# Optimization experiments

Hardware: AMD Instinct MI355X
Metric: run time of the kernel (lower is better)

## Reference

```python
import jax, jax.numpy as jnp
import numpy as np

N_NODES = 8192
N_EDGES = 131072

_DIMS = [
    ("cnn1", 3, 32), ("cnn2", 32, 64), ("cnn3", 64, 128),
    ("gcn1", 128, 256), ("gcn2", 256, 512), ("gcn3", 512, 1024),
    ("cnnd1", 1024, 512), ("cnnd2", 512, 256), ("cnnd3", 256, 128), ("cnnd4", 128, 50),
]


def setup_inputs() -> dict:
    key = jax.random.key(0)
    ks = jax.random.split(key, 2 + 2 * len(_DIMS))
    inp = {
        "x": jax.random.normal(ks[0], (N_NODES, 3), dtype=jnp.float32),
        "edge_index": jax.random.randint(ks[1], (2, N_EDGES), 0, N_NODES, dtype=jnp.int64)
        if jax.config.jax_enable_x64 else
        jax.random.randint(ks[1], (2, N_EDGES), 0, N_NODES, dtype=jnp.int32),
    }
    for i, (name, din, dout) in enumerate(_DIMS):
        scale = 1.0 / np.sqrt(din)
        inp[name + "_w"] = jax.random.normal(ks[2 + 2 * i], (din, dout), dtype=jnp.float32) * scale
        inp[name + "_b"] = jax.random.normal(ks[3 + 2 * i], (dout,), dtype=jnp.float32) * scale
    return inp


def _gcn_norm(edge_index, n, dtype):
    # add self-loops, symmetric normalization D^{-1/2}(A+I)D^{-1/2}
    loop = jnp.arange(n, dtype=edge_index.dtype)
    src = jnp.concatenate([edge_index[0], loop])
    dst = jnp.concatenate([edge_index[1], loop])
    deg = jax.ops.segment_sum(jnp.ones_like(dst, dtype=dtype), dst, num_segments=n)
    dinv = jnp.where(deg > 0, 1.0 / jnp.sqrt(deg), 0.0)
    norm = dinv[src] * dinv[dst]  # [E+N]
    return src, dst, norm


def _forward(x, edge_index,
             cnn1_w, cnn1_b, cnn2_w, cnn2_b, cnn3_w, cnn3_b,
             gcn1_w, gcn1_b, gcn2_w, gcn2_b, gcn3_w, gcn3_b,
             cnnd1_w, cnnd1_b, cnnd2_w, cnnd2_b, cnnd3_w, cnnd3_b, cnnd4_w, cnnd4_b):
    n = x.shape[0]
    src, dst, norm = _gcn_norm(edge_index, n, x.dtype)

    def lin(h, w, b):  # 1x1 Conv1d == per-node linear
        return h @ w + b

    def gcn(h, w, b):
        hl = h @ w                                    # [N, out]
        msg = hl[src] * norm[:, None]                 # gather + scale [E+N, out]
        return jax.ops.segment_sum(msg, dst, num_segments=n) + b

    h = jax.nn.relu(lin(x, cnn1_w, cnn1_b))
    h = jax.nn.relu(lin(h, cnn2_w, cnn2_b))
    h = jax.nn.relu(lin(h, cnn3_w, cnn3_b))
    h = jax.nn.relu(gcn(h, gcn1_w, gcn1_b))
    h = jax.nn.relu(gcn(h, gcn2_w, gcn2_b))
    h = jax.nn.relu(gcn(h, gcn3_w, gcn3_b))
    h = jax.nn.relu(lin(h, cnnd1_w, cnnd1_b))
    h = jax.nn.relu(lin(h, cnnd2_w, cnnd2_b))
    h = jax.nn.relu(lin(h, cnnd3_w, cnnd3_b))
    h = lin(h, cnnd4_w, cnnd4_b)
    return jax.nn.softmax(h, axis=1)  # [N, output_dim]


def reference(x, edge_index,
              cnn1_w, cnn1_b, cnn2_w, cnn2_b, cnn3_w, cnn3_b,
              gcn1_w, gcn1_b, gcn2_w, gcn2_b, gcn3_w, gcn3_b,
              cnnd1_w, cnnd1_b, cnnd2_w, cnnd2_b, cnnd3_w, cnnd3_b, cnnd4_w, cnnd4_b):
    return _forward(x, edge_index,
                    cnn1_w, cnn1_b, cnn2_w, cnn2_b, cnn3_w, cnn3_b,
                    gcn1_w, gcn1_b, gcn2_w, gcn2_b, gcn3_w, gcn3_b,
                    cnnd1_w, cnnd1_b, cnnd2_w, cnnd2_b, cnnd3_w, cnnd3_b, cnnd4_w, cnnd4_b)
```

## Files before the change

### kernel.cpp

```cpp
#include <hip/hip_runtime.h>
#include <math.h>

#define N_NODES 8192
#define N_EDGES 131072

typedef unsigned short u16;
typedef unsigned int u32;
typedef short bf16x8 __attribute__((ext_vector_type(8)));
typedef int v4i __attribute__((ext_vector_type(4)));
typedef float f32x4 __attribute__((ext_vector_type(4)));

__device__ __forceinline__ u16 f2bf(float x) {
    unsigned u = __float_as_uint(x);
    u += 0x7fffu + ((u >> 16) & 1u);
    return (u16)(u >> 16);
}
__device__ __forceinline__ float bf2f(u16 h) { return __uint_as_float(((unsigned)h) << 16); }

#define GLD_LDS(gp, lp) __builtin_amdgcn_global_load_lds( \
    (const __attribute__((address_space(1))) void*)(gp),  \
    (__attribute__((address_space(3))) void*)(lp), 16, 0, 0)

template <int N> __device__ __forceinline__ void wait_vmcnt() {
    if constexpr (N == 0) asm volatile("s_waitcnt vmcnt(0)" ::: "memory");
    else if constexpr (N == 8) asm volatile("s_waitcnt vmcnt(8)" ::: "memory");
    else static_assert(N < 0, "unsupported vmcnt");
}

__device__ __forceinline__ u32 lds_addr(const void* p) {
    return (u32)(size_t)(const __attribute__((address_space(3))) void*)p;
}

__device__ __forceinline__ bf16x8 lds_read_b128(u32 addr) {
    v4i r;
    asm volatile("ds_read_b128 %0, %1" : "=v"(r) : "v"(addr));
    union { v4i i; bf16x8 b; } u;
    u.i = r;
    return u.b;
}

template <int NU> struct UV;
template <> struct UV<1> { typedef u32 T; };
template <> struct UV<2> { typedef uint2 T; };
template <> struct UV<4> { typedef uint4 T; };


__global__ void k_zero_deg(int* __restrict__ deg) {
    int i = blockIdx.x * 256 + threadIdx.x;
    if (i < N_NODES) deg[i] = 0;
}

__global__ void k_count(const int* __restrict__ ei, int* __restrict__ deg) {
    int e = blockIdx.x * 256 + threadIdx.x;
    if (e < N_EDGES) atomicAdd(&deg[ei[N_EDGES + e]], 1);
}

__global__ __launch_bounds__(1024) void k_scan(const int* __restrict__ deg,
                                               int* __restrict__ rowptr,
                                               int* __restrict__ pos,
                                               float* __restrict__ dinv) {
    __shared__ int sums[1024];
    int t = threadIdx.x;
    int local[8];
    int s = 0;
#pragma unroll
    for (int i = 0; i < 8; ++i) {
        local[i] = deg[t * 8 + i];
        dinv[t * 8 + i] = 1.0f / sqrtf((float)(local[i] + 1));
        s += local[i];
    }
    sums[t] = s;
    __syncthreads();
    for (int off = 1; off < 1024; off <<= 1) {
        int v = (t >= off) ? sums[t - off] : 0;
        __syncthreads();
        sums[t] += v;
        __syncthreads();
    }
    int run = sums[t] - s;
#pragma unroll
    for (int i = 0; i < 8; ++i) {
        rowptr[t * 8 + i] = run;
        pos[t * 8 + i] = run;
        run += local[i];
    }
    if (t == 1023) rowptr[8192] = run;
}

__global__ void k_fill(const int* __restrict__ ei, const float* __restrict__ dinv,
                       int* __restrict__ pos, int* __restrict__ csr_src,
                       float* __restrict__ csr_w) {
    int e = blockIdx.x * 256 + threadIdx.x;
    if (e < N_EDGES) {
        int s = ei[e];
        int t = ei[N_EDGES + e];
        int idx = atomicAdd(&pos[t], 1);
        csr_src[idx] = s;
        csr_w[idx] = dinv[s] * dinv[t];
    }
}

__global__ void k_prep_all(const float* __restrict__ g1w, const float* __restrict__ g2w,
                           const float* __restrict__ g3w, const float* __restrict__ d1w,
                           const float* __restrict__ d2w, const float* __restrict__ d3w,
                           u16* __restrict__ wts) {
    int idx = blockIdx.x * 256 + threadIdx.x;
    const float* W;
    int local, lgK, N;
    u16 *hi, *lo;
    if (idx < 32768)        { W = g1w; local = idx;           lgK = 7;  N = 256;  hi = wts;           lo = wts + 32768; }
    else if (idx < 163840)  { W = g2w; local = idx - 32768;   lgK = 8;  N = 512;  hi = wts + 65536;   lo = wts + 196608; }
    else if (idx < 688128)  { W = g3w; local = idx - 163840;  lgK = 9;  N = 1024; hi = wts + 327680;  lo = wts + 851968; }
    else if (idx < 1212416) { W = d1w; local = idx - 688128;  lgK = 10; N = 512;  hi = wts + 1376256; lo = wts + 1900544; }
    else if (idx < 1343488) { W = d2w; local = idx - 1212416; lgK = 9;  N = 256;  hi = wts + 2424832; lo = wts + 2555904; }
    else if (idx < 1376256) { W = d3w; local = idx - 1343488; lgK = 8;  N = 128;  hi = wts + 2686976; lo = wts + 2719744; }
    else return;
    int n = local >> lgK;
    int k = local & ((1 << lgK) - 1);
    float v = W[(size_t)k * N + n];
    u16 h = f2bf(v);
    hi[local] = h;
    lo[local] = f2bf(v - bf2f(h));
}

__global__ __launch_bounds__(256) void k_enc_fused(const float* __restrict__ x,
                                                   const float* __restrict__ w1, const float* __restrict__ b1,
                                                   const float* __restrict__ w2, const float* __restrict__ b2,
                                                   const float* __restrict__ w3, const float* __restrict__ b3,
                                                   u16* __restrict__ Chi, u16* __restrict__ Clo) {
    __shared__ float lw[10560];
    const int tid = threadIdx.x;
    for (int i = tid; i < 96; i += 256) lw[i] = w1[i];
    for (int i = tid; i < 32; i += 256) lw[96 + i] = b1[i];
    for (int i = tid; i < 2048; i += 256) lw[128 + i] = w2[i];
    for (int i = tid; i < 64; i += 256) lw[2176 + i] = b2[i];
    for (int i = tid; i < 8192; i += 256) lw[2240 + i] = w3[i];
    for (int i = tid; i < 128; i += 256) lw[10432 + i] = b3[i];
    __syncthreads();

    const int lane = tid & 63;
    const int node = blockIdx.x * 4 + (tid >> 6);

    float x0 = x[node * 3 + 0], x1 = x[node * 3 + 1], x2 = x[node * 3 + 2];

    int o1 = lane & 31;
    float h1 = fmaxf(x0 * lw[o1] + x1 * lw[32 + o1] + x2 * lw[64 + o1] + lw[96 + o1], 0.f);

    float h2 = lw[2176 + lane];
#pragma unroll
    for (int k = 0; k < 32; ++k) h2 += __shfl(h1, k) * lw[128 + k * 64 + lane];
    h2 = fmaxf(h2, 0.f);

    float h3a = lw[10432 + lane];
    float h3b = lw[10432 + 64 + lane];
#pragma unroll
    for (int k = 0; k < 64; ++k) {
        float hk = __shfl(h2, k);
        h3a += hk * lw[2240 + k * 128 + lane];
        h3b += hk * lw[2240 + k * 128 + 64 + lane];
    }
    h3a = fmaxf(h3a, 0.f);
    h3b = fmaxf(h3b, 0.f);

    size_t base = (size_t)node * 128;
    u16 ha = f2bf(h3a), hb = f2bf(h3b);
    Chi[base + lane] = ha;
    Chi[base + 64 + lane] = hb;
    Clo[base + lane] = f2bf(h3a - bf2f(ha));
    Clo[base + 64 + lane] = f2bf(h3b - bf2f(hb));
}

__global__ __launch_bounds__(256) void k_d4sm_fused(const float* __restrict__ A,
                                                    const float* __restrict__ W,
                                                    const float* __restrict__ bias,
                                                    float* __restrict__ out) {
    __shared__ float lw[6450];
    const int tid = threadIdx.x;
    for (int i = tid; i < 6400; i += 256) lw[i] = W[i];
    for (int i = tid; i < 50; i += 256) lw[6400 + i] = bias[i];
    __syncthreads();

    const int lane = tid & 63;
    const int node = blockIdx.x * 4 + (tid >> 6);

    float a0 = A[(size_t)node * 128 + lane];
    float a1 = A[(size_t)node * 128 + 64 + lane];

    float acc = (lane < 50) ? lw[6400 + lane] : 0.f;
    int oc = (lane < 50) ? lane : 0;
#pragma unroll
    for (int k = 0; k < 64; ++k) acc += __shfl(a0, k) * lw[k * 50 + oc];
#pragma unroll
    for (int k = 0; k < 64; ++k) acc += __shfl(a1, k) * lw[(64 + k) * 50 + oc];

    float v = (lane < 50) ? acc : -INFINITY;
    float m = v;
#pragma unroll
    for (int off = 32; off; off >>= 1) m = fmaxf(m, __shfl_xor(m, off));
    float e = (lane < 50) ? expf(v - m) : 0.f;
    float s = e;
#pragma unroll
    for (int off = 32; off; off >>= 1) s += __shfl_xor(s, off);
    if (lane < 50) out[(size_t)node * 50 + lane] = e / s;
}

template <int D>
__global__ __launch_bounds__(256) void k_agg_s(const u16* __restrict__ hi_in,
                                               const u16* __restrict__ lo_in,
                                               u16* __restrict__ hi_out,
                                               u16* __restrict__ lo_out,
                                               const int* __restrict__ rowptr,
                                               const int* __restrict__ csr_src,
                                               const float* __restrict__ csr_w,
                                               const float* __restrict__ dinv) {
    constexpr int EPL = D / 64;
    constexpr int NU = EPL / 2;
    using VT = typename UV<NU>::T;
    int node = blockIdx.x * 4 + (threadIdx.x >> 6);
    int lane = threadIdx.x & 63;
    const size_t off = (size_t)node * D + lane * EPL;
    float acc[EPL];
    {
        float dn = dinv[node];
        float w0 = dn * dn;
        u32 hu[NU], lu[NU];
        *(VT*)hu = *(const VT*)(hi_in + off);
        *(VT*)lu = *(const VT*)(lo_in + off);
#pragma unroll
        for (int j = 0; j < NU; ++j) {
            acc[2 * j]     = (__uint_as_float(hu[j] << 16) + __uint_as_float(lu[j] << 16)) * w0;
            acc[2 * j + 1] = (__uint_as_float(hu[j] & 0xffff0000u) + __uint_as_float(lu[j] & 0xffff0000u)) * w0;
        }
    }
#define EDGE_ACC(S, W) do {                                                            \
        size_t so = (size_t)(S) * D + lane * EPL;                                      \
        u32 hu[NU], lu[NU];                                                            \
        *(VT*)hu = *(const VT*)(hi_in + so);                                           \
        *(VT*)lu = *(const VT*)(lo_in + so);                                           \
        _Pragma("unroll")                                                              \
        for (int j = 0; j < NU; ++j) {                                                 \
            acc[2 * j]     += (__uint_as_float(hu[j] << 16) + __uint_as_float(lu[j] << 16)) * (W); \
            acc[2 * j + 1] += (__uint_as_float(hu[j] & 0xffff0000u) + __uint_as_float(lu[j] & 0xffff0000u)) * (W); \
        }                                                                              \
    } while (0)
    int beg = rowptr[node], end = rowptr[node + 1];
    int e = beg;
    for (; e + 2 <= end; e += 2) {
        int s0 = csr_src[e], s1 = csr_src[e + 1];
        float wa = csr_w[e], wb = csr_w[e + 1];
        EDGE_ACC(s0, wa);
        EDGE_ACC(s1, wb);
    }
    if (e < end) EDGE_ACC(csr_src[e], csr_w[e]);
#undef EDGE_ACC
    u32 how[NU], low[NU];
#pragma unroll
    for (int j = 0; j < NU; ++j) {
        u16 h0 = f2bf(acc[2 * j]);     u16 l0 = f2bf(acc[2 * j] - bf2f(h0));
        u16 h1 = f2bf(acc[2 * j + 1]); u16 l1 = f2bf(acc[2 * j + 1] - bf2f(h1));
        how[j] = (u32)h0 | ((u32)h1 << 16);
        low[j] = (u32)l0 | ((u32)l1 << 16);
    }
    *(VT*)(hi_out + off) = *(VT*)how;
    *(VT*)(lo_out + off) = *(VT*)low;
}

template <int D>
__global__ __launch_bounds__(256) void k_agg(const float* __restrict__ h, float* __restrict__ out,
                                             const int* __restrict__ rowptr,
                                             const int* __restrict__ csr_src,
                                             const float* __restrict__ csr_w,
                                             const float* __restrict__ dinv) {
    constexpr int NF2 = D / 128;
    int node = blockIdx.x * 4 + (threadIdx.x >> 6);
    int lane = threadIdx.x & 63;
    const float2* hn = (const float2*)(h + (size_t)node * D);
    float dn = dinv[node];
    float w0 = dn * dn;
    float2 acc[NF2];
#pragma unroll
    for (int j = 0; j < NF2; ++j) {
        float2 v = hn[lane + j * 64];
        acc[j].x = v.x * w0;
        acc[j].y = v.y * w0;
    }
    int beg = rowptr[node], end = rowptr[node + 1];
    for (int e = beg; e < end; ++e) {
        int s = csr_src[e];
        float w = csr_w[e];
        const float2* hs = (const float2*)(h + (size_t)s * D);
#pragma unroll
        for (int j = 0; j < NF2; ++j) {
            float2 v = hs[lane + j * 64];
            acc[j].x += v.x * w;
            acc[j].y += v.y * w;
        }
    }
    float2* op = (float2*)(out + (size_t)node * D);
#pragma unroll
    for (int j = 0; j < NF2; ++j) op[lane + j * 64] = acc[j];
}

template <int OUTS>
__global__ __launch_bounds__(64) void k_linear_small(const float* __restrict__ A,
                                                     const float* __restrict__ W,
                                                     const float* __restrict__ bias,
                                                     float* __restrict__ Cf,
                                                     u16* __restrict__ Chi,
                                                     u16* __restrict__ Clo,
                                                     int K, int N, int relu) {
    int n = blockIdx.y;
    int o = blockIdx.x * 64 + threadIdx.x;
    if (o >= N) return;
    float s = bias[o];
    const float* a = A + (size_t)n * K;
    for (int k = 0; k < K; ++k) s += a[k] * W[(size_t)k * N + o];
    if (relu) s = fmaxf(s, 0.0f);
    if (OUTS == 0) {
        Cf[(size_t)n * N + o] = s;
    } else {
        u16 h = f2bf(s);
        Chi[(size_t)n * N + o] = h;
        Clo[(size_t)n * N + o] = f2bf(s - bf2f(h));
    }
}

template <int OUTS>
__global__ __launch_bounds__(256, 2) void k_gemm_mfma(
    const u16* __restrict__ Ahi, const u16* __restrict__ Alo,
    const u16* __restrict__ Bhi, const u16* __restrict__ Blo,
    const float* __restrict__ bias,
    float* __restrict__ Cf, u16* __restrict__ Chi, u16* __restrict__ Clo,
    int M, int N, int K, int relu) {
    constexpr int BM = 128, BN = 128, WM = 64, WN = 64;
    constexpr int BK = 32;
    constexpr int NW_N = BN / WN;
    constexpr int FM = WM / 16, FN = WN / 16;
    constexpr int ASZ = (BK / 8) * BM * 16;
    constexpr int BSZ = (BK / 8) * BN * 16;
    constexpr int TOT = 2 * ASZ + 2 * BSZ;
    constexpr int NSTG = TOT / 4096;

    __shared__ char lds0[TOT] __attribute__((aligned(16)));
    __shared__ char lds1[TOT] __attribute__((aligned(16)));

    const int tid = threadIdx.x;
    const int lane = tid & 63;
    const int wave = tid >> 6;
    const int wy = wave / NW_N, wx = wave % NW_N;

    const int nwg = gridDim.x * gridDim.y;
    const int d = blockIdx.y * gridDim.x + blockIdx.x;
    const int q = nwg >> 3;
    const int lg = (d & 7) * q + (d >> 3);
    const int bx = lg % gridDim.x, by = lg / gridDim.x;
    const int m0 = by * BM, n0 = bx * BN;

    const u16* gp[NSTG];
    int ldo[NSTG];
#pragma unroll
    for (int i = 0; i < NSTG; ++i) {
        int o = i * 4096 + tid * 16;
        ldo[i] = o;
        const u16* base;
        int roff, rows, org;
        if (o < ASZ)                { base = Ahi; roff = o;                 rows = BM; org = m0; }
        else if (o < 2 * ASZ)       { base = Alo; roff = o - ASZ;           rows = BM; org = m0; }
        else if (o < 2 * ASZ + BSZ) { base = Bhi; roff = o - 2 * ASZ;       rows = BN; org = n0; }
        else                        { base = Blo; roff = o - 2 * ASZ - BSZ; rows = BN; org = n0; }
        int c = roff / (rows * 16);
        int r = (roff % (rows * 16)) / 16;
        gp[i] = base + (size_t)(org + r) * K + c * 8;
    }

    const int kc = lane >> 4, rr = lane & 15;
    const int aoff = (kc * BM + wy * WM + rr) * 16;
    const int boff = 2 * ASZ + (kc * BN + wx * WN + rr) * 16;

    f32x4 acc[FM][FN];
#pragma unroll
    for (int i = 0; i < FM; ++i)
#pragma unroll
        for (int j = 0; j < FN; ++j) acc[i][j] = f32x4{0.f, 0.f, 0.f, 0.f};

#define STAGE(P, KS) do {                                          \
        _Pragma("unroll")                                          \
        for (int i = 0; i < NSTG; ++i)                             \
            GLD_LDS(gp[i] + (KS) * BK, (P) + ldo[i]);              \
    } while (0)

#define STEP(CUR, DST, KS) do {                                                     \
        wait_vmcnt<0>();                                                            \
        asm volatile("s_barrier" ::: "memory");                                     \
        if ((KS) + 1 < nks) STAGE(DST, (KS) + 1);                                   \
        const u32 pb_ = lds_addr(CUR);                                              \
        bf16x8 ah[FM], al[FM], bh[FN], bl[FN];                                      \
        _Pragma("unroll")                                                           \
        for (int fm = 0; fm < FM; ++fm) {                                           \
            ah[fm] = lds_read_b128(pb_ + aoff + fm * 256);                          \
            al[fm] = lds_read_b128(pb_ + ASZ + aoff + fm * 256);                    \
        }                                                                           \
        _Pragma("unroll")                                                           \
        for (int fn = 0; fn < FN; ++fn) {                                           \
            bh[fn] = lds_read_b128(pb_ + boff + fn * 256);                          \
            bl[fn] = lds_read_b128(pb_ + BSZ + boff + fn * 256);                    \
        }                                                                           \
        asm volatile("s_waitcnt lgkmcnt(0)");                                       \
        __builtin_amdgcn_sched_barrier(0);                                          \
        __builtin_amdgcn_s_setprio(1);                                              \
        _Pragma("unroll")                                                           \
        for (int fm = 0; fm < FM; ++fm)                                             \
            _Pragma("unroll")                                                       \
            for (int fn = 0; fn < FN; ++fn) {                                       \
                acc[fm][fn] = __builtin_amdgcn_mfma_f32_16x16x32_bf16(ah[fm], bh[fn], acc[fm][fn], 0, 0, 0); \
                acc[fm][fn] = __builtin_amdgcn_mfma_f32_16x16x32_bf16(al[fm], bh[fn], acc[fm][fn], 0, 0, 0); \
                acc[fm][fn] = __builtin_amdgcn_mfma_f32_16x16x32_bf16(ah[fm], bl[fn], acc[fm][fn], 0, 0, 0); \
            }                                                                       \
        __builtin_amdgcn_s_setprio(0);                                              \
    } while (0)

    const int nks = K / BK;
    STAGE(lds0, 0);
    for (int base = 0; base < nks; base += 2) {
        STEP(lds0, lds1, base);
        STEP(lds1, lds0, base + 1);
    }
    asm volatile("" ::: "memory");
#undef STEP
#undef STAGE

    const int cr = (lane >> 4) * 4;
    const int cc = lane & 15;
#pragma unroll
    for (int fm = 0; fm < FM; ++fm)
#pragma unroll
        for (int fn = 0; fn < FN; ++fn) {
            int col = n0 + wx * WN + fn * 16 + cc;
            float bv = bias[col];
#pragma unroll
            for (int r = 0; r < 4; ++r) {
                int row = m0 + wy * WM + fm * 16 + cr + r;
                float v = acc[fm][fn][r] + bv;
                if (relu) v = fmaxf(v, 0.f);
                if (OUTS == 0) {
                    Cf[(size_t)row * N + col] = v;
                } else {
                    u16 h = f2bf(v);
                    Chi[(size_t)row * N + col] = h;
                    Clo[(size_t)row * N + col] = f2bf(v - bf2f(h));
                }
            }
        }
}

template <int BM, int BN, int BK, int TM, int TN>
__global__ __launch_bounds__(256) void k_gemm(const float* __restrict__ A,
                                              const float* __restrict__ W,
                                              const float* __restrict__ bias,
                                              float* __restrict__ C,
                                              int M, int N, int K, int relu) {
    constexpr int TX = BN / TN;
    constexpr int TY = BM / TM;
    __shared__ float As[BK][BM + 4];
    __shared__ float Bs[BK][BN];
    int tid = threadIdx.x;
    int tx = tid % TX, ty = tid / TX;
    int m0 = blockIdx.y * BM, n0 = blockIdx.x * BN;
    float acc[TM][TN] = {};
    for (int k0 = 0; k0 < K; k0 += BK) {
        for (int v = tid; v < BM * BK / 4; v += TX * TY) {
            int r = v / (BK / 4);
            int kcp = (v % (BK / 4)) * 4;
            float4 val = *(const float4*)&A[(size_t)(m0 + r) * K + k0 + kcp];
            As[kcp + 0][r] = val.x; As[kcp + 1][r] = val.y;
            As[kcp + 2][r] = val.z; As[kcp + 3][r] = val.w;
        }
        for (int v = tid; v < BK * BN / 4; v += TX * TY) {
            int kr = v / (BN / 4);
            int c = (v % (BN / 4)) * 4;
            *(float4*)&Bs[kr][c] = *(const float4*)&W[(size_t)(k0 + kr) * N + n0 + c];
        }
        __syncthreads();
#pragma unroll
        for (int kk = 0; kk < BK; ++kk) {
            float a[TM], b[TN];
#pragma unroll
            for (int i = 0; i < TM; i += 4) {
                float4 t4 = *(const float4*)&As[kk][ty * TM + i];
                a[i] = t4.x; a[i + 1] = t4.y; a[i + 2] = t4.z; a[i + 3] = t4.w;
            }
#pragma unroll
            for (int j = 0; j < TN; j += 4) {
                float4 t4 = *(const float4*)&Bs[kk][tx * TN + j];
                b[j] = t4.x; b[j + 1] = t4.y; b[j + 2] = t4.z; b[j + 3] = t4.w;
            }
#pragma unroll
            for (int i = 0; i < TM; ++i)
#pragma unroll
                for (int j = 0; j < TN; ++j) acc[i][j] += a[i] * b[j];
        }
        __syncthreads();
    }
#pragma unroll
    for (int i = 0; i < TM; ++i) {
        int row = m0 + ty * TM + i;
#pragma unroll
        for (int j = 0; j < TN; j += 4) {
            int col = n0 + tx * TN + j;
            float4 v;
            v.x = acc[i][j + 0] + bias[col + 0];
            v.y = acc[i][j + 1] + bias[col + 1];
            v.z = acc[i][j + 2] + bias[col + 2];
            v.w = acc[i][j + 3] + bias[col + 3];
            if (relu) {
                v.x = fmaxf(v.x, 0.0f); v.y = fmaxf(v.y, 0.0f);
                v.z = fmaxf(v.z, 0.0f); v.w = fmaxf(v.w, 0.0f);
            }
            *(float4*)&C[(size_t)row * N + col] = v;
        }
    }
}

__global__ __launch_bounds__(256) void k_softmax50(const float* __restrict__ in,
                                                   float* __restrict__ out) {
    int row = blockIdx.x * 4 + (threadIdx.x >> 6);
    int lane = threadIdx.x & 63;
    float v = (lane < 50) ? in[(size_t)row * 50 + lane] : -INFINITY;
    float m = v;
#pragma unroll
    for (int off = 32; off; off >>= 1) m = fmaxf(m, __shfl_xor(m, off));
    float e = (lane < 50) ? expf(v - m) : 0.0f;
    float s = e;
#pragma unroll
    for (int off = 32; off; off >>= 1) s += __shfl_xor(s, off);
    if (lane < 50) out[(size_t)row * 50 + lane] = e / s;
}


extern "C" void kernel_launch(void* const* d_in, const int* in_sizes, int n_in,
                              void* d_out, int out_size, void* d_ws, size_t ws_size,
                              hipStream_t stream) {
    const float* x  = (const float*)d_in[0];
    const int*   ei = (const int*)d_in[1];
    const float *w1  = (const float*)d_in[2],  *b1  = (const float*)d_in[3];
    const float *w2  = (const float*)d_in[4],  *b2  = (const float*)d_in[5];
    const float *w3  = (const float*)d_in[6],  *b3  = (const float*)d_in[7];
    const float *g1w = (const float*)d_in[8],  *g1b = (const float*)d_in[9];
    const float *g2w = (const float*)d_in[10], *g2b = (const float*)d_in[11];
    const float *g3w = (const float*)d_in[12], *g3b = (const float*)d_in[13];
    const float *d1w = (const float*)d_in[14], *d1b = (const float*)d_in[15];
    const float *d2w = (const float*)d_in[16], *d2b = (const float*)d_in[17];
    const float *d3w = (const float*)d_in[18], *d3b = (const float*)d_in[19];
    const float *d4w = (const float*)d_in[20], *d4b = (const float*)d_in[21];
    float* out = (float*)d_out;

    const size_t NEED_NEW = 57016576ull;

    if (ws_size >= NEED_NEW) {
        char* w = (char*)d_ws;
        u16* p0hi = (u16*)w;
        u16* p0lo = (u16*)(w + 16777216);
        u16* p1hi = (u16*)(w + 33554432);
        u16* p1lo = (u16*)(w + 41943040);
        float* f0 = (float*)p1hi;
        u16* wts = (u16*)(w + 50331648);
        u16 *wt1h = wts,            *wt1l = wt1h + 32768;
        u16 *wt2h = wt1l + 32768,   *wt2l = wt2h + 131072;
        u16 *wt3h = wt2l + 131072,  *wt3l = wt3h + 524288;
        u16 *wd1h = wt3l + 524288,  *wd1l = wd1h + 524288;
        u16 *wd2h = wd1l + 524288,  *wd2l = wd2h + 131072;
        u16 *wd3h = wd2l + 131072,  *wd3l = wd3h + 32768;
        char* cs = w + 55836672;
        int*   deg     = (int*)cs;
        int*   rowptr  = deg + N_NODES;
        int*   pos     = rowptr + 8256;
        float* dinv    = (float*)(pos + N_NODES);
        int*   csr_src = (int*)(dinv + N_NODES);
        float* csr_w   = (float*)(csr_src + N_EDGES);

        k_zero_deg<<<N_NODES / 256, 256, 0, stream>>>(deg);
        k_count<<<N_EDGES / 256, 256, 0, stream>>>(ei, deg);
        k_scan<<<1, 1024, 0, stream>>>(deg, rowptr, pos, dinv);
        k_fill<<<N_EDGES / 256, 256, 0, stream>>>(ei, dinv, pos, csr_src, csr_w);

        k_prep_all<<<1376256 / 256, 256, 0, stream>>>(g1w, g2w, g3w, d1w, d2w, d3w, wts);

        k_enc_fused<<<N_NODES / 4, 256, 0, stream>>>(x, w1, b1, w2, b2, w3, b3, p0hi, p0lo);

        k_agg_s<128><<<N_NODES / 4, 256, 0, stream>>>(p0hi, p0lo, p1hi, p1lo, rowptr, csr_src, csr_w, dinv);
        k_gemm_mfma<1><<<dim3(256 / 128, N_NODES / 128), 256, 0, stream>>>(
            p1hi, p1lo, wt1h, wt1l, g1b, nullptr, p0hi, p0lo, N_NODES, 256, 128, 1);
        k_agg_s<256><<<N_NODES / 4, 256, 0, stream>>>(p0hi, p0lo, p1hi, p1lo, rowptr, csr_src, csr_w, dinv);
        k_gemm_mfma<1><<<dim3(512 / 128, N_NODES / 128), 256, 0, stream>>>(
            p1hi, p1lo, wt2h, wt2l, g2b, nullptr, p0hi, p0lo, N_NODES, 512, 256, 1);
        k_agg_s<512><<<N_NODES / 4, 256, 0, stream>>>(p0hi, p0lo, p1hi, p1lo, rowptr, csr_src, csr_w, dinv);
        k_gemm_mfma<1><<<dim3(1024 / 128, N_NODES / 128), 256, 0, stream>>>(
            p1hi, p1lo, wt3h, wt3l, g3b, nullptr, p0hi, p0lo, N_NODES, 1024, 512, 1);
        k_gemm_mfma<1><<<dim3(512 / 128, N_NODES / 128), 256, 0, stream>>>(
            p0hi, p0lo, wd1h, wd1l, d1b, nullptr, p1hi, p1lo, N_NODES, 512, 1024, 1);
        k_gemm_mfma<1><<<dim3(256 / 128, N_NODES / 128), 256, 0, stream>>>(
            p1hi, p1lo, wd2h, wd2l, d2b, nullptr, p0hi, p0lo, N_NODES, 256, 512, 1);
        k_gemm_mfma<0><<<dim3(128 / 128, N_NODES / 128), 256, 0, stream>>>(
            p0hi, p0lo, wd3h, wd3l, d3b, f0, nullptr, nullptr, N_NODES, 128, 256, 1);

        k_d4sm_fused<<<N_NODES / 4, 256, 0, stream>>>(f0, d4w, d4b, out);
    } else {
        float* bufA = (float*)d_ws;
        float* bufB = bufA + (size_t)N_NODES * 1024;
        int*   deg     = (int*)(bufB + (size_t)N_NODES * 512);
        int*   rowptr  = deg + N_NODES;
        int*   pos     = rowptr + 8256;
        float* dinv    = (float*)(pos + N_NODES);
        int*   csr_src = (int*)(dinv + N_NODES);
        float* csr_w   = (float*)(csr_src + N_EDGES);

        k_zero_deg<<<N_NODES / 256, 256, 0, stream>>>(deg);
        k_count<<<N_EDGES / 256, 256, 0, stream>>>(ei, deg);
        k_scan<<<1, 1024, 0, stream>>>(deg, rowptr, pos, dinv);
        k_fill<<<N_EDGES / 256, 256, 0, stream>>>(ei, dinv, pos, csr_src, csr_w);

        k_linear_small<0><<<dim3(1, N_NODES), 64, 0, stream>>>(x,    w1, b1, bufA, nullptr, nullptr, 3, 32, 1);
        k_linear_small<0><<<dim3(1, N_NODES), 64, 0, stream>>>(bufA, w2, b2, bufB, nullptr, nullptr, 32, 64, 1);
        k_linear_small<0><<<dim3(2, N_NODES), 64, 0, stream>>>(bufB, w3, b3, bufA, nullptr, nullptr, 64, 128, 1);

        k_agg<128><<<N_NODES / 4, 256, 0, stream>>>(bufA, bufB, rowptr, csr_src, csr_w, dinv);
        k_gemm<64, 64, 16, 4, 4><<<dim3(256 / 64, N_NODES / 64), 256, 0, stream>>>(
            bufB, g1w, g1b, bufA, N_NODES, 256, 128, 1);
        k_agg<256><<<N_NODES / 4, 256, 0, stream>>>(bufA, bufB, rowptr, csr_src, csr_w, dinv);
        k_gemm<128, 128, 16, 8, 8><<<dim3(512 / 128, N_NODES / 128), 256, 0, stream>>>(
            bufB, g2w, g2b, bufA, N_NODES, 512, 256, 1);
        k_agg<512><<<N_NODES / 4, 256, 0, stream>>>(bufA, bufB, rowptr, csr_src, csr_w, dinv);
        k_gemm<128, 128, 16, 8, 8><<<dim3(1024 / 128, N_NODES / 128), 256, 0, stream>>>(
            bufB, g3w, g3b, bufA, N_NODES, 1024, 512, 1);
        k_gemm<128, 128, 16, 8, 8><<<dim3(512 / 128, N_NODES / 128), 256, 0, stream>>>(
            bufA, d1w, d1b, bufB, N_NODES, 512, 1024, 1);
        k_gemm<64, 64, 16, 4, 4><<<dim3(256 / 64, N_NODES / 64), 256, 0, stream>>>(
            bufB, d2w, d2b, bufA, N_NODES, 256, 512, 1);
        k_gemm<64, 64, 16, 4, 4><<<dim3(128 / 64, N_NODES / 64), 256, 0, stream>>>(
            bufA, d3w, d3b, bufB, N_NODES, 128, 256, 1);
        k_linear_small<0><<<dim3(1, N_NODES), 64, 0, stream>>>(bufB, d4w, d4b, bufA, nullptr, nullptr, 128, 50, 0);
        k_softmax50<<<N_NODES / 4, 256, 0, stream>>>(bufA, out);
    }
}
```

Before: 309.3 us.

## Load GEMM B operand directly from global into registers with pre-swizzled layout

The weight conversion kernel now writes the hi/lo bf16 weights in an MFMA-fragment-friendly interleaved layout (k-chunks of 8 contiguous per output column). The GEMM stops staging B through LDS and instead loads B fragments straight from global memory into double-buffered registers one k-step ahead. This halves the LDS footprint and LDS read traffic and removes B from the barrier-synchronised staging path. In exchange it raises register pressure and relies on the vmcnt ordering so the A staging and the B register prefetch stay correct. Each wave also re-reads B from global/L2 rather than sharing one copy per block.

```diff
diff --git a/kernel.cpp b/kernel.cpp
--- a/kernel.cpp
+++ b/kernel.cpp
@@ -119,8 +119,9 @@
     int k = local & ((1 << lgK) - 1);
     float v = W[(size_t)k * N + n];
     u16 h = f2bf(v);
-    hi[local] = h;
-    lo[local] = f2bf(v - bf2f(h));
+    int dst = ((k >> 3) * N + n) * 8 + (k & 7);
+    hi[dst] = h;
+    lo[dst] = f2bf(v - bf2f(h));
 }
 
 __global__ __launch_bounds__(256) void k_enc_fused(const float* __restrict__ x,
@@ -337,8 +338,7 @@
     constexpr int NW_N = BN / WN;
     constexpr int FM = WM / 16, FN = WN / 16;
     constexpr int ASZ = (BK / 8) * BM * 16;
-    constexpr int BSZ = (BK / 8) * BN * 16;
-    constexpr int TOT = 2 * ASZ + 2 * BSZ;
+    constexpr int TOT = 2 * ASZ;
     constexpr int NSTG = TOT / 4096;
 
     __shared__ char lds0[TOT] __attribute__((aligned(16)));
@@ -363,25 +363,27 @@
         int o = i * 4096 + tid * 16;
         ldo[i] = o;
         const u16* base;
-        int roff, rows, org;
-        if (o < ASZ)                { base = Ahi; roff = o;                 rows = BM; org = m0; }
-        else if (o < 2 * ASZ)       { base = Alo; roff = o - ASZ;           rows = BM; org = m0; }
-        else if (o < 2 * ASZ + BSZ) { base = Bhi; roff = o - 2 * ASZ;       rows = BN; org = n0; }
-        else                        { base = Blo; roff = o - 2 * ASZ - BSZ; rows = BN; org = n0; }
-        int c = roff / (rows * 16);
-        int r = (roff % (rows * 16)) / 16;
-        gp[i] = base + (size_t)(org + r) * K + c * 8;
+        int roff;
+        if (o < ASZ) { base = Ahi; roff = o; }
+        else         { base = Alo; roff = o - ASZ; }
+        int c = roff / (BM * 16);
+        int r = (roff % (BM * 16)) / 16;
+        gp[i] = base + (size_t)(m0 + r) * K + c * 8;
     }
 
     const int kc = lane >> 4, rr = lane & 15;
     const int aoff = (kc * BM + wy * WM + rr) * 16;
-    const int boff = 2 * ASZ + (kc * BN + wx * WN + rr) * 16;
+
+    const size_t bbase = ((size_t)kc * N + n0 + wx * WN + rr) * 8;
+    const size_t bstep = (size_t)4 * N * 8;
 
     f32x4 acc[FM][FN];
 #pragma unroll
     for (int i = 0; i < FM; ++i)
 #pragma unroll
         for (int j = 0; j < FN; ++j) acc[i][j] = f32x4{0.f, 0.f, 0.f, 0.f};
+
+    bf16x8 b0h[FN], b0l[FN], b1h[FN], b1l[FN];
 
 #define STAGE(P, KS) do {                                          \
         _Pragma("unroll")                                          \
@@ -389,21 +391,26 @@
             GLD_LDS(gp[i] + (KS) * BK, (P) + ldo[i]);              \
     } while (0)
 
-#define STEP(CUR, DST, KS) do {                                                     \
-        wait_vmcnt<0>();                                                            \
+#define LOADB(BH, BL, KS) do {                                                      \
+        _Pragma("unroll")                                                           \
+        for (int fn = 0; fn < FN; ++fn) {                                           \
+            BH[fn] = *(const bf16x8*)(Bhi + bbase + (size_t)(KS) * bstep + fn * 128); \
+            BL[fn] = *(const bf16x8*)(Blo + bbase + (size_t)(KS) * bstep + fn * 128); \
+        }                                                                           \
+    } while (0)
+
+#define STEP(CUR, DST, BHC, BLC, BHD, BLD, KS) do {                                 \
+        if ((KS) + 1 < nks) LOADB(BHD, BLD, (KS) + 1);                              \
+        __builtin_amdgcn_sched_barrier(0);                                          \
+        if ((KS) + 1 < nks) wait_vmcnt<8>(); else wait_vmcnt<0>();                  \
         asm volatile("s_barrier" ::: "memory");                                     \
         if ((KS) + 1 < nks) STAGE(DST, (KS) + 1);                                   \
         const u32 pb_ = lds_addr(CUR);                                              \
-        bf16x8 ah[FM], al[FM], bh[FN], bl[FN];                                      \
+        bf16x8 ah[FM], al[FM];                                                      \
         _Pragma("unroll")                                                           \
         for (int fm = 0; fm < FM; ++fm) {                                           \
             ah[fm] = lds_read_b128(pb_ + aoff + fm * 256);                          \
             al[fm] = lds_read_b128(pb_ + ASZ + aoff + fm * 256);                    \
-        }                                                                           \
-        _Pragma("unroll")                                                           \
-        for (int fn = 0; fn < FN; ++fn) {                                           \
-            bh[fn] = lds_read_b128(pb_ + boff + fn * 256);                          \
-            bl[fn] = lds_read_b128(pb_ + BSZ + boff + fn * 256);                    \
         }                                                                           \
         asm volatile("s_waitcnt lgkmcnt(0)");                                       \
         __builtin_amdgcn_sched_barrier(0);                                          \
@@ -412,21 +419,23 @@
         for (int fm = 0; fm < FM; ++fm)                                             \
             _Pragma("unroll")                                                       \
             for (int fn = 0; fn < FN; ++fn) {                                       \
-                acc[fm][fn] = __builtin_amdgcn_mfma_f32_16x16x32_bf16(ah[fm], bh[fn], acc[fm][fn], 0, 0, 0); \
-                acc[fm][fn] = __builtin_amdgcn_mfma_f32_16x16x32_bf16(al[fm], bh[fn], acc[fm][fn], 0, 0, 0); \
-                acc[fm][fn] = __builtin_amdgcn_mfma_f32_16x16x32_bf16(ah[fm], bl[fn], acc[fm][fn], 0, 0, 0); \
+                acc[fm][fn] = __builtin_amdgcn_mfma_f32_16x16x32_bf16(ah[fm], BHC[fn], acc[fm][fn], 0, 0, 0); \
+                acc[fm][fn] = __builtin_amdgcn_mfma_f32_16x16x32_bf16(al[fm], BHC[fn], acc[fm][fn], 0, 0, 0); \
+                acc[fm][fn] = __builtin_amdgcn_mfma_f32_16x16x32_bf16(ah[fm], BLC[fn], acc[fm][fn], 0, 0, 0); \
             }                                                                       \
         __builtin_amdgcn_s_setprio(0);                                              \
     } while (0)
 
     const int nks = K / BK;
+    LOADB(b0h, b0l, 0);
     STAGE(lds0, 0);
     for (int base = 0; base < nks; base += 2) {
-        STEP(lds0, lds1, base);
-        STEP(lds1, lds0, base + 1);
+        STEP(lds0, lds1, b0h, b0l, b1h, b1l, base);
+        STEP(lds1, lds0, b1h, b1l, b0h, b0l, base + 1);
     }
     asm volatile("" ::: "memory");
 #undef STEP
+#undef LOADB
 #undef STAGE
 
     const int cr = (lane >> 4) * 4;
```

After: 291.2 us. -5.9%, faster.
